# Kernel optimization log

Measured on AMD Instinct MI355X. Metric: run time of the kernel, lower is better.

Reference implementation:

```python
import jax, jax.numpy as jnp
import numpy as np

FREQ = 129  # STFT_FILTERS // 2


def conv1d(x, w, b, stride, pad):
    # x: [B, Cin, L], w: [Cout, Cin, K] (torch Conv1d layout)
    out = jax.lax.conv_general_dilated(x, w, (stride,), [(pad, pad)],
                                       dimension_numbers=('NCH', 'OIH', 'NCH'))
    if b is not None:
        out = out + b[None, :, None]
    return out


def setup_inputs() -> dict:
    key = jax.random.key(0)
    ks = jax.random.split(key, 17)
    B = 16384
    s = 0.05
    return {
        'x': jax.random.normal(ks[0], (B, 512), jnp.float32),
        'state': jax.random.normal(ks[1], (2, B, 128), jnp.float32),
        'stft_w': jax.random.normal(ks[2], (258, 1, 256), jnp.float32) * s,
        'w1': jax.random.normal(ks[3], (128, 129, 3), jnp.float32) * s,
        'b1': jax.random.normal(ks[4], (128,), jnp.float32) * s,
        'w2': jax.random.normal(ks[5], (64, 128, 3), jnp.float32) * s,
        'b2': jax.random.normal(ks[6], (64,), jnp.float32) * s,
        'w3': jax.random.normal(ks[7], (64, 64, 3), jnp.float32) * s,
        'b3': jax.random.normal(ks[8], (64,), jnp.float32) * s,
        'w4': jax.random.normal(ks[9], (128, 64, 3), jnp.float32) * s,
        'b4': jax.random.normal(ks[10], (128,), jnp.float32) * s,
        'w_ih': jax.random.normal(ks[11], (512, 128), jnp.float32) * s,
        'w_hh': jax.random.normal(ks[12], (512, 128), jnp.float32) * s,
        'b_ih': jax.random.normal(ks[13], (512,), jnp.float32) * s,
        'b_hh': jax.random.normal(ks[14], (512,), jnp.float32) * s,
        'fw': jax.random.normal(ks[15], (1, 128, 1), jnp.float32) * s,
        'fb': jax.random.normal(ks[16], (1,), jnp.float32) * s,
    }


def reference(x, state, stft_w, w1, b1, w2, b2, w3, b3, w4, b4,
              w_ih, w_hh, b_ih, b_hh, fw, fb):
    # reflect-pad right by 64: [B, 512] -> [B, 576], add channel dim
    xp = jnp.pad(x, ((0, 0), (0, 64)), mode='reflect')[:, None, :]
    s = conv1d(xp, stft_w, None, 128, 0)            # [B, 258, 3]
    real, imag = s[:, :FREQ], s[:, FREQ:]
    h = jnp.sqrt(real * real + imag * imag)          # magnitude [B, 129, 3]
    h = jax.nn.relu(conv1d(h, w1, b1, 1, 1))         # [B, 128, 3]
    h = jax.nn.relu(conv1d(h, w2, b2, 2, 1))         # [B, 64, 2]
    h = jax.nn.relu(conv1d(h, w3, b3, 2, 1))         # [B, 64, 1]
    h = jax.nn.relu(conv1d(h, w4, b4, 1, 1))         # [B, 128, 1]
    feat = h[:, :, 0]                                # [B, 128]
    # torch LSTMCell: gate order i, f, g, o
    gates = feat @ w_ih.T + b_ih + state[0] @ w_hh.T + b_hh
    i, f, g, o = jnp.split(gates, 4, axis=1)
    c = jax.nn.sigmoid(f) * state[1] + jax.nn.sigmoid(i) * jnp.tanh(g)
    hn = jax.nn.sigmoid(o) * jnp.tanh(c)
    new_state = jnp.stack([hn, c], axis=0)           # [2, B, 128]
    z = jax.nn.relu(hn)[:, :, None]                  # [B, 128, 1]
    z = jax.nn.sigmoid(conv1d(z, fw, fb, 1, 0))      # [B, 1, 1]
    out = z[:, 0].mean(axis=1, keepdims=True)        # [B, 1]
    return out, new_state
```

## Files before the change

### kernel.cpp

```cpp
#include <hip/hip_runtime.h>
#include <math.h>

typedef unsigned short ushort_t;
typedef short short8 __attribute__((ext_vector_type(8)));
typedef float floatx4 __attribute__((ext_vector_type(4)));

#define MFMA16(a,b,c) __builtin_amdgcn_mfma_f32_16x16x32_bf16((a),(b),(c),0,0,0)

#define PK_STFT 0
#define PK_W1   69632
#define PK_W2   131072
#define PK_W3   155648
#define PK_W4   167936
#define PK_LSTM 176128
#define OFF_MAG 307200
#define OFF_FEAT 8171520

__device__ __forceinline__ ushort_t f2bf(float f){
    unsigned int u = __float_as_uint(f);
    u += 0x7fffu + ((u >> 16) & 1u);
    return (ushort_t)(u >> 16);
}
__device__ __forceinline__ float bf2f(ushort_t h){
    return __uint_as_float(((unsigned int)h) << 16);
}
__device__ __forceinline__ unsigned int pack2(float a, float b){
    return (unsigned int)f2bf(a) | ((unsigned int)f2bf(b) << 16);
}
__device__ __forceinline__ float fsig(float v){
    return __builtin_amdgcn_rcpf(1.f + __builtin_amdgcn_exp2f(-1.44269504f * v));
}
__device__ __forceinline__ float ftanh(float v){
    return 2.f * __builtin_amdgcn_rcpf(1.f + __builtin_amdgcn_exp2f(-2.88539008f * v)) - 1.f;
}

__global__ __launch_bounds__(256) void prep_kernel(
    const float* __restrict__ stft_w, const float* __restrict__ w1,
    const float* __restrict__ w2, const float* __restrict__ w3,
    const float* __restrict__ w4, const float* __restrict__ wih,
    const float* __restrict__ whh, ushort_t* __restrict__ wp)
{
    int i = blockIdx.x * 256 + threadIdx.x;
    if (i >= 307200) return;
    float val = 0.f;
    if (i < PK_W1) {
        int frag = i >> 9, rr = i & 511, l = rr >> 3, j = rr & 7;
        int ct = frag >> 3, kk = frag & 7;
        int kd = kk * 32 + ((l >> 4) << 3) + j;
        int n = ct * 16 + (l & 15);
        val = (n < 258) ? stft_w[n * 256 + kd] : 0.f;
    } else if (i < PK_W2) {
        int r = i - PK_W1;
        int tap = r / 20480; r -= tap * 20480;
        int frag = r >> 9, rr = r & 511, l = rr >> 3, j = rr & 7;
        int ct = frag / 5, kk = frag - ct * 5;
        int kd = kk * 32 + ((l >> 4) << 3) + j;
        int c = ct * 16 + (l & 15);
        val = (kd < 129) ? w1[c * 387 + kd * 3 + tap] : 0.f;
    } else if (i < PK_W3) {
        int r = i - PK_W2;
        int frag = r >> 9, rr = r & 511, l = rr >> 3, j = rr & 7;
        int ct = frag / 12, kk = frag - ct * 12;
        int kd = kk * 32 + ((l >> 4) << 3) + j;
        int k = kd >> 7, f = kd & 127;
        int c = ct * 16 + (l & 15);
        val = w2[c * 384 + f * 3 + k];
    } else if (i < PK_W4) {
        int r = i - PK_W3;
        int frag = r >> 9, rr = r & 511, l = rr >> 3, j = rr & 7;
        int ct = frag / 6, kk = frag - ct * 6;
        int kd = kk * 32 + ((l >> 4) << 3) + j;
        int k = kd >> 6, f = kd & 63;
        int c = ct * 16 + (l & 15);
        val = w3[c * 192 + f * 3 + k];
    } else if (i < PK_LSTM) {
        int r = i - PK_W4;
        int frag = r >> 9, rr = r & 511, l = rr >> 3, j = rr & 7;
        int ct = frag >> 1, kk = frag & 1;
        int kd = kk * 32 + ((l >> 4) << 3) + j;
        int c = ct * 16 + (l & 15);
        val = w4[c * 192 + kd * 3 + 1];
    } else {
        int r = i - PK_LSTM;
        int frag = r >> 9, rr = r & 511, l = rr >> 3, j = rr & 7;
        int ct = frag >> 3, kk = frag & 7;
        int kd = kk * 32 + ((l >> 4) << 3) + j;
        int n = ct * 16 + (l & 15);
        val = (kd < 128) ? wih[n * 128 + kd] : whh[n * 128 + (kd - 128)];
    }
    wp[i] = f2bf(val);
}

__global__ __launch_bounds__(256) void stft_kernel(
    const float* __restrict__ x, const ushort_t* __restrict__ wp,
    ushort_t* __restrict__ magg)
{
    __shared__ ushort_t xs[48 * 264];
    __shared__ ushort_t s[48 * 264];
    const int tid = threadIdx.x, lane = tid & 63, wid = tid >> 6;
    const int l15 = lane & 15, lk = lane >> 4;

    {
        const float4* xg = (const float4*)(x + (size_t)blockIdx.x * 16 * 512);
#pragma unroll
        for (int i = 0; i < 8; ++i) {
            int idx4 = tid + i * 256;
            float4 v = xg[idx4];
            int b = idx4 >> 7, c4 = idx4 & 127;
            int si = c4 * 4, t1 = si >> 7;
            unsigned int u0 = pack2(v.x, v.y), u1 = pack2(v.z, v.w);
            if (t1 < 3) {
                ushort_t* p = &xs[(b * 3 + t1) * 264 + (si & 127)];
                *(unsigned int*)p = u0; *(unsigned int*)(p + 2) = u1;
            }
            if (t1 >= 1) {
                ushort_t* p = &xs[(b * 3 + t1 - 1) * 264 + (si & 127) + 128];
                *(unsigned int*)p = u0; *(unsigned int*)(p + 2) = u1;
            }
        }
    }
    __syncthreads();

    for (int ct = wid; ct < 17; ct += 4) {
        short8 bfrag[8];
        const short8* bp = (const short8*)(wp + PK_STFT) + (size_t)(ct * 8) * 64 + lane;
#pragma unroll
        for (int kk = 0; kk < 8; ++kk) bfrag[kk] = bp[kk * 64];
        int col = ct * 16 + l15;
#pragma unroll
        for (int rt = 0; rt < 3; ++rt) {
            const ushort_t* abase = &xs[(rt * 16 + l15) * 264 + lk * 8];
            floatx4 acc = {0.f, 0.f, 0.f, 0.f};
#pragma unroll
            for (int kk = 0; kk < 8; ++kk) {
                short8 af = *(const short8*)(abase + kk * 32);
                acc = MFMA16(af, bfrag[kk], acc);
            }
            if (col < 258) {
                int r0 = rt * 16 + lk * 4;
#pragma unroll
                for (int jj = 0; jj < 4; ++jj) s[(r0 + jj) * 264 + col] = f2bf(acc[jj]);
            }
        }
    }
    __syncthreads();

    {
        size_t ob = (size_t)blockIdx.x * 16 * 480;
        for (int idx = tid; idx < 48 * 129; idx += 256) {
            int bt = idx / 129, f = idx - bt * 129;
            float re = bf2f(s[bt * 264 + f]);
            float im = bf2f(s[bt * 264 + 129 + f]);
            int b = bt / 3, t = bt - b * 3;
            magg[ob + b * 480 + t * 160 + f] = f2bf(sqrtf(re * re + im * im));
        }
        for (int idx = tid; idx < 48 * 31; idx += 256) {
            int bt = idx / 31, f = 129 + (idx - bt * 31);
            int b = bt / 3, t = bt - b * 3;
            magg[ob + b * 480 + t * 160 + f] = 0;
        }
    }
}

__global__ __launch_bounds__(256) void conv_kernel(
    const ushort_t* __restrict__ wp, const ushort_t* __restrict__ magg,
    const float* __restrict__ b1, const float* __restrict__ b2,
    const float* __restrict__ b3, const float* __restrict__ b4,
    ushort_t* __restrict__ featg)
{
    __shared__ ushort_t big[13440];
    __shared__ ushort_t h2h[16 * 3 * 72];
    __shared__ ushort_t h3s[16 * 72];
    const int tid = threadIdx.x, lane = tid & 63, wid = tid >> 6;
    const int l15 = lane & 15, lk = lane >> 4;

    {
        unsigned int* bz = (unsigned int*)big;
        for (int i = tid; i < 2688; i += 256) {
            int bb = i / 168, r = i - bb * 168;
            int tp = (r < 84) ? 0 : 4, f2 = (r < 84) ? r : r - 84;
            bz[(bb * 5 + tp) * 84 + f2] = 0u;
        }
        for (int i = tid; i < 576; i += 256) {
            int bb = i / 36, f2 = i - bb * 36;
            ((unsigned int*)h2h)[bb * 108 + f2] = 0u;
        }
        const unsigned int* mg = (const unsigned int*)(magg + (size_t)blockIdx.x * 16 * 480);
        for (int i = tid; i < 3840; i += 256) {
            int bb = i / 240, r = i - bb * 240;
            int t = r / 80, f2 = r - t * 80;
            bz[(bb * 5 + 1 + t) * 84 + f2] = mg[i];
        }
    }
    __syncthreads();

    floatx4 acc1[2][3];
#pragma unroll
    for (int ci = 0; ci < 2; ++ci)
#pragma unroll
        for (int rt = 0; rt < 3; ++rt) acc1[ci][rt] = (floatx4){0.f, 0.f, 0.f, 0.f};
#pragma unroll
    for (int ci = 0; ci < 2; ++ci) {
        int ct = wid + ci * 4;
        short8 bfrag[15];
#pragma unroll
        for (int tap = 0; tap < 3; ++tap)
#pragma unroll
            for (int kk = 0; kk < 5; ++kk)
                bfrag[tap * 5 + kk] = ((const short8*)(wp + PK_W1))[(size_t)(tap * 40 + ct * 5 + kk) * 64 + lane];
#pragma unroll
        for (int rt = 0; rt < 3; ++rt) {
            int obt = rt * 16 + l15;
            int b = obt / 3, t = obt - b * 3;
#pragma unroll
            for (int tap = 0; tap < 3; ++tap) {
                const ushort_t* abase = &big[(b * 5 + t + tap) * 168 + lk * 8];
#pragma unroll
                for (int kk = 0; kk < 5; ++kk) {
                    short8 af = *(const short8*)(abase + kk * 32);
                    acc1[ci][rt] = MFMA16(af, bfrag[tap * 5 + kk], acc1[ci][rt]);
                }
            }
        }
    }
    __syncthreads();

    {
        unsigned int* h1z = (unsigned int*)big;
        for (int i = tid; i < 2176; i += 256) {
            int bb = i / 136, r = i - bb * 136;
            int tp = (r < 68) ? 0 : 4, f2 = (r < 68) ? r : r - 68;
            h1z[(bb * 5 + tp) * 68 + f2] = 0u;
        }
#pragma unroll
        for (int ci = 0; ci < 2; ++ci) {
            int ct = wid + ci * 4;
            int col = ct * 16 + l15;
            float bias = b1[col];
#pragma unroll
            for (int rt = 0; rt < 3; ++rt)
#pragma unroll
                for (int jj = 0; jj < 4; ++jj) {
                    int obt = rt * 16 + lk * 4 + jj;
                    int b = obt / 3, t = obt - b * 3;
                    big[(b * 5 + t + 1) * 136 + col] = f2bf(fmaxf(acc1[ci][rt][jj] + bias, 0.f));
                }
        }
    }
    __syncthreads();

    {
        int ct = wid;
        short8 bfrag[12];
#pragma unroll
        for (int kk = 0; kk < 12; ++kk)
            bfrag[kk] = ((const short8*)(wp + PK_W2))[(size_t)(ct * 12 + kk) * 64 + lane];
        int col = ct * 16 + l15;
        float bias = b2[col];
#pragma unroll
        for (int rt = 0; rt < 2; ++rt) {
            floatx4 acc = {0.f, 0.f, 0.f, 0.f};
            int orow = rt * 16 + l15;
            int b = orow >> 1, t2 = orow & 1;
#pragma unroll
            for (int kk = 0; kk < 12; ++kk) {
                int k = kk >> 2, f = (kk & 3) * 32 + lk * 8;
                short8 af = *(const short8*)(&big[(b * 5 + 2 * t2 + k) * 136 + f]);
                acc = MFMA16(af, bfrag[kk], acc);
            }
#pragma unroll
            for (int jj = 0; jj < 4; ++jj) {
                int orw = rt * 16 + lk * 4 + jj;
                int bb = orw >> 1, tt = orw & 1;
                h2h[(bb * 3 + 1 + tt) * 72 + col] = f2bf(fmaxf(acc[jj] + bias, 0.f));
            }
        }
    }
    __syncthreads();

    {
        int ct = wid;
        short8 bfrag[6];
#pragma unroll
        for (int kk = 0; kk < 6; ++kk)
            bfrag[kk] = ((const short8*)(wp + PK_W3))[(size_t)(ct * 6 + kk) * 64 + lane];
        int col = ct * 16 + l15;
        float bias = b3[col];
        floatx4 acc = {0.f, 0.f, 0.f, 0.f};
        int b = l15;
#pragma unroll
        for (int kk = 0; kk < 6; ++kk) {
            int k = kk >> 1, f = (kk & 1) * 32 + lk * 8;
            short8 af = *(const short8*)(&h2h[(b * 3 + k) * 72 + f]);
            acc = MFMA16(af, bfrag[kk], acc);
        }
#pragma unroll
        for (int jj = 0; jj < 4; ++jj) {
            int bb = lk * 4 + jj;
            h3s[bb * 72 + col] = f2bf(fmaxf(acc[jj] + bias, 0.f));
        }
    }
    __syncthreads();

    {
#pragma unroll
        for (int ci = 0; ci < 2; ++ci) {
            int ct = wid + ci * 4;
            short8 bf0 = ((const short8*)(wp + PK_W4))[(size_t)(ct * 2 + 0) * 64 + lane];
            short8 bf1 = ((const short8*)(wp + PK_W4))[(size_t)(ct * 2 + 1) * 64 + lane];
            int col = ct * 16 + l15;
            float bias = b4[col];
            floatx4 acc = {0.f, 0.f, 0.f, 0.f};
            int b = l15;
            short8 a0 = *(const short8*)(&h3s[b * 72 + lk * 8]);
            short8 a1 = *(const short8*)(&h3s[b * 72 + 32 + lk * 8]);
            acc = MFMA16(a0, bf0, acc);
            acc = MFMA16(a1, bf1, acc);
#pragma unroll
            for (int jj = 0; jj < 4; ++jj) {
                int bb = lk * 4 + jj;
                featg[((size_t)blockIdx.x * 16 + bb) * 128 + col] = f2bf(fmaxf(acc[jj] + bias, 0.f));
            }
        }
    }
}

__global__ __launch_bounds__(512) void lstm_kernel(
    const ushort_t* __restrict__ featg, const float* __restrict__ state,
    const ushort_t* __restrict__ wp, const float* __restrict__ bih,
    const float* __restrict__ bhh, const float* __restrict__ fw,
    const float* __restrict__ fbp, float* __restrict__ out, int B)
{
    __shared__ ushort_t inc[32 * 264];
    __shared__ float red[256];
    const int tid = threadIdx.x, lane = tid & 63, wid = tid >> 6;
    const int l15 = lane & 15, lk = lane >> 4;
    const size_t b0 = (size_t)blockIdx.x * 32;
    const int cc = wid * 16 + l15;

    const float* cprev = state + (size_t)B * 128;
    float cpv[2][4];
#pragma unroll
    for (int rt = 0; rt < 2; ++rt)
#pragma unroll
        for (int jj = 0; jj < 4; ++jj)
            cpv[rt][jj] = cprev[(b0 + rt * 16 + lk * 4 + jj) * 128 + cc];

    {
        const unsigned int* fg = (const unsigned int*)(featg + b0 * 128);
        unsigned int* ip = (unsigned int*)inc;
        for (int i = tid; i < 2048; i += 512) {
            int bb = i >> 6, f2 = i & 63;
            ip[bb * 132 + f2] = fg[i];
        }
        const float* hp = state + b0 * 128;
        for (int i = tid; i < 2048; i += 512) {
            int bb = i >> 6, c2 = i & 63;
            float2 v = *(const float2*)&hp[bb * 128 + c2 * 2];
            ip[bb * 132 + 64 + c2] = pack2(v.x, v.y);
        }
    }
    __syncthreads();

    floatx4 acc[4][2];
#pragma unroll
    for (int ci = 0; ci < 4; ++ci) {
        int ct = wid + ci * 8;
        short8 bfrag[8];
#pragma unroll
        for (int kk = 0; kk < 8; ++kk)
            bfrag[kk] = ((const short8*)(wp + PK_LSTM))[(size_t)(ct * 8 + kk) * 64 + lane];
#pragma unroll
        for (int rt = 0; rt < 2; ++rt) {
            const ushort_t* abase = &inc[(rt * 16 + l15) * 264 + lk * 8];
            floatx4 a = {0.f, 0.f, 0.f, 0.f};
#pragma unroll
            for (int kk = 0; kk < 8; ++kk) {
                short8 af = *(const short8*)(abase + kk * 32);
                a = MFMA16(af, bfrag[kk], a);
            }
            acc[ci][rt] = a;
        }
    }

    float* outh = out + B;
    float* outc = out + B + (size_t)B * 128;
    float ph[2][4];
    const float bi = bih[cc] + bhh[cc];
    const float bf_ = bih[cc + 128] + bhh[cc + 128];
    const float bg = bih[cc + 256] + bhh[cc + 256];
    const float bo = bih[cc + 384] + bhh[cc + 384];
    const float fwv = fw[cc];
#pragma unroll
    for (int rt = 0; rt < 2; ++rt)
#pragma unroll
        for (int jj = 0; jj < 4; ++jj) {
            int row = rt * 16 + lk * 4 + jj;
            size_t gb = b0 + row;
            float gi = acc[0][rt][jj] + bi;
            float gf = acc[1][rt][jj] + bf_;
            float gg = acc[2][rt][jj] + bg;
            float go = acc[3][rt][jj] + bo;
            float cn = fsig(gf) * cpv[rt][jj] + fsig(gi) * ftanh(gg);
            float hn = fsig(go) * ftanh(cn);
            outh[gb * 128 + cc] = hn;
            outc[gb * 128 + cc] = cn;
            ph[rt][jj] = fmaxf(hn, 0.f) * fwv;
        }

#pragma unroll
    for (int rt = 0; rt < 2; ++rt)
#pragma unroll
        for (int jj = 0; jj < 4; ++jj) {
            float v = ph[rt][jj];
            v += __shfl_xor(v, 1, 64);
            v += __shfl_xor(v, 2, 64);
            v += __shfl_xor(v, 4, 64);
            v += __shfl_xor(v, 8, 64);
            if (l15 == 0) red[wid * 32 + rt * 16 + lk * 4 + jj] = v;
        }
    __syncthreads();
    if (tid < 32) {
        float v = 0.f;
#pragma unroll
        for (int w = 0; w < 8; ++w) v += red[w * 32 + tid];
        out[b0 + tid] = fsig(v + fbp[0]);
    }
}

extern "C" void kernel_launch(void* const* d_in, const int* in_sizes, int n_in,
                              void* d_out, int out_size, void* d_ws, size_t ws_size,
                              hipStream_t stream) {
    const float* x      = (const float*)d_in[0];
    const float* state  = (const float*)d_in[1];
    const float* stft_w = (const float*)d_in[2];
    const float* w1     = (const float*)d_in[3];
    const float* b1     = (const float*)d_in[4];
    const float* w2     = (const float*)d_in[5];
    const float* b2     = (const float*)d_in[6];
    const float* w3     = (const float*)d_in[7];
    const float* b3     = (const float*)d_in[8];
    const float* w4     = (const float*)d_in[9];
    const float* b4     = (const float*)d_in[10];
    const float* wih    = (const float*)d_in[11];
    const float* whh    = (const float*)d_in[12];
    const float* bih    = (const float*)d_in[13];
    const float* bhh    = (const float*)d_in[14];
    const float* fw     = (const float*)d_in[15];
    const float* fbp    = (const float*)d_in[16];

    ushort_t* wp = (ushort_t*)d_ws;
    const int B = in_sizes[0] / 512;

    prep_kernel<<<1200, 256, 0, stream>>>(stft_w, w1, w2, w3, w4, wih, whh, wp);
    stft_kernel<<<B / 16, 256, 0, stream>>>(x, wp, wp + OFF_MAG);
    conv_kernel<<<B / 16, 256, 0, stream>>>(wp, wp + OFF_MAG, b1, b2, b3, b4, wp + OFF_FEAT);
    lstm_kernel<<<B / 32, 512, 0, stream>>>(wp + OFF_FEAT, state, wp, bih, bhh, fw, fbp,
                                            (float*)d_out, B);
}
```

Baseline: 73.69 us.

## Fuse STFT, conv stack and LSTM into one per-16-row kernel

Merges the three separate kernels (STFT magnitude, conv stack, LSTM cell) into one block-per-16-batch-rows kernel. Magnitude and feature intermediates stay in shared memory instead of going through global workspace buffers. The previous hidden and cell state are prefetched into registers before the STFT work starts. This removes global round trips and two launches, but the kernel uses more registers and LDS (launch bounds set to 3 blocks per SM). The LSTM GEMM now runs per 16-row tile with half the batch rows per block, so its weight fragments are reloaded twice as often.

```diff
diff --git a/kernel.cpp b/kernel.cpp
--- a/kernel.cpp
+++ b/kernel.cpp
@@ -13,8 +13,6 @@
 #define PK_W3   155648
 #define PK_W4   167936
 #define PK_LSTM 176128
-#define OFF_MAG 307200
-#define OFF_FEAT 8171520
 
 __device__ __forceinline__ ushort_t f2bf(float f){
     unsigned int u = __float_as_uint(f);
@@ -91,17 +89,26 @@
     wp[i] = f2bf(val);
 }
 
-__global__ __launch_bounds__(256) void stft_kernel(
-    const float* __restrict__ x, const ushort_t* __restrict__ wp,
-    ushort_t* __restrict__ magg)
+__global__ __launch_bounds__(256, 3) void fused_kernel(
+    const float* __restrict__ x, const float* __restrict__ state,
+    const ushort_t* __restrict__ wp,
+    const float* __restrict__ b1, const float* __restrict__ b2,
+    const float* __restrict__ b3, const float* __restrict__ b4,
+    const float* __restrict__ bih, const float* __restrict__ bhh,
+    const float* __restrict__ fw, const float* __restrict__ fbp,
+    float* __restrict__ out, int B)
 {
-    __shared__ ushort_t xs[48 * 264];
-    __shared__ ushort_t s[48 * 264];
+    __shared__ ushort_t A[12672];
+    __shared__ ushort_t Bb[13440];
+    __shared__ float red[64];
+
     const int tid = threadIdx.x, lane = tid & 63, wid = tid >> 6;
     const int l15 = lane & 15, lk = lane >> 4;
-
-    {
-        const float4* xg = (const float4*)(x + (size_t)blockIdx.x * 16 * 512);
+    const size_t b0 = (size_t)blockIdx.x * 16;
+
+    for (int i = tid; i < 6720; i += 256) ((unsigned int*)Bb)[i] = 0u;
+    {
+        const float4* xg = (const float4*)(x + b0 * 512);
 #pragma unroll
         for (int i = 0; i < 8; ++i) {
             int idx4 = tid + i * 256;
@@ -110,87 +117,87 @@
             int si = c4 * 4, t1 = si >> 7;
             unsigned int u0 = pack2(v.x, v.y), u1 = pack2(v.z, v.w);
             if (t1 < 3) {
-                ushort_t* p = &xs[(b * 3 + t1) * 264 + (si & 127)];
+                ushort_t* p = &A[(b * 3 + t1) * 264 + (si & 127)];
                 *(unsigned int*)p = u0; *(unsigned int*)(p + 2) = u1;
             }
             if (t1 >= 1) {
-                ushort_t* p = &xs[(b * 3 + t1 - 1) * 264 + (si & 127) + 128];
+                ushort_t* p = &A[(b * 3 + t1 - 1) * 264 + (si & 127) + 128];
                 *(unsigned int*)p = u0; *(unsigned int*)(p + 2) = u1;
             }
         }
     }
-    __syncthreads();
-
-    for (int ct = wid; ct < 17; ct += 4) {
-        short8 bfrag[8];
-        const short8* bp = (const short8*)(wp + PK_STFT) + (size_t)(ct * 8) * 64 + lane;
-#pragma unroll
-        for (int kk = 0; kk < 8; ++kk) bfrag[kk] = bp[kk * 64];
-        int col = ct * 16 + l15;
-#pragma unroll
-        for (int rt = 0; rt < 3; ++rt) {
-            const ushort_t* abase = &xs[(rt * 16 + l15) * 264 + lk * 8];
-            floatx4 acc = {0.f, 0.f, 0.f, 0.f};
-#pragma unroll
-            for (int kk = 0; kk < 8; ++kk) {
-                short8 af = *(const short8*)(abase + kk * 32);
-                acc = MFMA16(af, bfrag[kk], acc);
-            }
+    unsigned int hpk[4];
+    {
+        const float* hp = state + b0 * 128;
+#pragma unroll
+        for (int k = 0; k < 4; ++k) {
+            int i = tid + k * 256;
+            int bb = i >> 6, c2 = i & 63;
+            float2 v = *(const float2*)&hp[bb * 128 + c2 * 2];
+            hpk[k] = pack2(v.x, v.y);
+        }
+    }
+    const float* cprev = state + (size_t)B * 128;
+    float cpv[2][4];
+#pragma unroll
+    for (int g2 = 0; g2 < 2; ++g2) {
+        int cc = (wid + g2 * 4) * 16 + l15;
+#pragma unroll
+        for (int jj = 0; jj < 4; ++jj)
+            cpv[g2][jj] = cprev[(b0 + lk * 4 + jj) * 128 + cc];
+    }
+    __syncthreads();
+
+    floatx4 accs[5][3];
+#pragma unroll
+    for (int ci = 0; ci < 5; ++ci)
+#pragma unroll
+        for (int rt = 0; rt < 3; ++rt) accs[ci][rt] = (floatx4){0.f, 0.f, 0.f, 0.f};
+#pragma unroll
+    for (int ci = 0; ci < 5; ++ci) {
+        int ct = wid + ci * 4;
+        if (ct < 17) {
+            short8 bfrag[8];
+            const short8* bp = (const short8*)(wp + PK_STFT) + (size_t)(ct * 8) * 64 + lane;
+#pragma unroll
+            for (int kk = 0; kk < 8; ++kk) bfrag[kk] = bp[kk * 64];
+#pragma unroll
+            for (int rt = 0; rt < 3; ++rt) {
+                const ushort_t* abase = &A[(rt * 16 + l15) * 264 + lk * 8];
+                floatx4 a = accs[ci][rt];
+#pragma unroll
+                for (int kk = 0; kk < 8; ++kk)
+                    a = MFMA16(*(const short8*)(abase + kk * 32), bfrag[kk], a);
+                accs[ci][rt] = a;
+            }
+        }
+    }
+    __syncthreads();
+
+#pragma unroll
+    for (int ci = 0; ci < 5; ++ci) {
+        int ct = wid + ci * 4;
+        if (ct < 17) {
+            int col = ct * 16 + l15;
             if (col < 258) {
-                int r0 = rt * 16 + lk * 4;
-#pragma unroll
-                for (int jj = 0; jj < 4; ++jj) s[(r0 + jj) * 264 + col] = f2bf(acc[jj]);
-            }
-        }
-    }
-    __syncthreads();
-
-    {
-        size_t ob = (size_t)blockIdx.x * 16 * 480;
-        for (int idx = tid; idx < 48 * 129; idx += 256) {
-            int bt = idx / 129, f = idx - bt * 129;
-            float re = bf2f(s[bt * 264 + f]);
-            float im = bf2f(s[bt * 264 + 129 + f]);
-            int b = bt / 3, t = bt - b * 3;
-            magg[ob + b * 480 + t * 160 + f] = f2bf(sqrtf(re * re + im * im));
-        }
-        for (int idx = tid; idx < 48 * 31; idx += 256) {
-            int bt = idx / 31, f = 129 + (idx - bt * 31);
-            int b = bt / 3, t = bt - b * 3;
-            magg[ob + b * 480 + t * 160 + f] = 0;
-        }
-    }
-}
-
-__global__ __launch_bounds__(256) void conv_kernel(
-    const ushort_t* __restrict__ wp, const ushort_t* __restrict__ magg,
-    const float* __restrict__ b1, const float* __restrict__ b2,
-    const float* __restrict__ b3, const float* __restrict__ b4,
-    ushort_t* __restrict__ featg)
-{
-    __shared__ ushort_t big[13440];
-    __shared__ ushort_t h2h[16 * 3 * 72];
-    __shared__ ushort_t h3s[16 * 72];
-    const int tid = threadIdx.x, lane = tid & 63, wid = tid >> 6;
-    const int l15 = lane & 15, lk = lane >> 4;
-
-    {
-        unsigned int* bz = (unsigned int*)big;
-        for (int i = tid; i < 2688; i += 256) {
-            int bb = i / 168, r = i - bb * 168;
-            int tp = (r < 84) ? 0 : 4, f2 = (r < 84) ? r : r - 84;
-            bz[(bb * 5 + tp) * 84 + f2] = 0u;
-        }
-        for (int i = tid; i < 576; i += 256) {
-            int bb = i / 36, f2 = i - bb * 36;
-            ((unsigned int*)h2h)[bb * 108 + f2] = 0u;
-        }
-        const unsigned int* mg = (const unsigned int*)(magg + (size_t)blockIdx.x * 16 * 480);
-        for (int i = tid; i < 3840; i += 256) {
-            int bb = i / 240, r = i - bb * 240;
-            int t = r / 80, f2 = r - t * 80;
-            bz[(bb * 5 + 1 + t) * 84 + f2] = mg[i];
-        }
+#pragma unroll
+                for (int rt = 0; rt < 3; ++rt) {
+                    int r0 = rt * 16 + lk * 4;
+#pragma unroll
+                    for (int jj = 0; jj < 4; ++jj)
+                        A[(r0 + jj) * 264 + col] = f2bf(accs[ci][rt][jj]);
+                }
+            }
+        }
+    }
+    __syncthreads();
+
+    for (int idx = tid; idx < 6192; idx += 256) {
+        int bt = idx / 129, f = idx - bt * 129;
+        float re = bf2f(A[bt * 264 + f]);
+        float im = bf2f(A[bt * 264 + 129 + f]);
+        int b = bt / 3, t = bt - b * 3;
+        Bb[b * 840 + (1 + t) * 168 + f] = f2bf(sqrtf(re * re + im * im));
     }
     __syncthreads();
 
@@ -214,28 +221,29 @@
             int b = obt / 3, t = obt - b * 3;
 #pragma unroll
             for (int tap = 0; tap < 3; ++tap) {
-                const ushort_t* abase = &big[(b * 5 + t + tap) * 168 + lk * 8];
-#pragma unroll
-                for (int kk = 0; kk < 5; ++kk) {
-                    short8 af = *(const short8*)(abase + kk * 32);
-                    acc1[ci][rt] = MFMA16(af, bfrag[tap * 5 + kk], acc1[ci][rt]);
-                }
-            }
-        }
-    }
-    __syncthreads();
-
-    {
-        unsigned int* h1z = (unsigned int*)big;
+                const ushort_t* abase = &Bb[(b * 5 + t + tap) * 168 + lk * 8];
+#pragma unroll
+                for (int kk = 0; kk < 5; ++kk)
+                    acc1[ci][rt] = MFMA16(*(const short8*)(abase + kk * 32), bfrag[tap * 5 + kk], acc1[ci][rt]);
+            }
+        }
+    }
+    __syncthreads();
+
+    {
+        unsigned int* h1z = (unsigned int*)A;
         for (int i = tid; i < 2176; i += 256) {
             int bb = i / 136, r = i - bb * 136;
             int tp = (r < 68) ? 0 : 4, f2 = (r < 68) ? r : r - 68;
             h1z[(bb * 5 + tp) * 68 + f2] = 0u;
         }
+        for (int i = tid; i < 576; i += 256) {
+            int bb = i / 36, f2 = i - bb * 36;
+            ((unsigned int*)Bb)[bb * 108 + f2] = 0u;
+        }
 #pragma unroll
         for (int ci = 0; ci < 2; ++ci) {
-            int ct = wid + ci * 4;
-            int col = ct * 16 + l15;
+            int ct = wid + ci * 4, col = ct * 16 + l15;
             float bias = b1[col];
 #pragma unroll
             for (int rt = 0; rt < 3; ++rt)
@@ -243,7 +251,7 @@
                 for (int jj = 0; jj < 4; ++jj) {
                     int obt = rt * 16 + lk * 4 + jj;
                     int b = obt / 3, t = obt - b * 3;
-                    big[(b * 5 + t + 1) * 136 + col] = f2bf(fmaxf(acc1[ci][rt][jj] + bias, 0.f));
+                    A[(b * 5 + t + 1) * 136 + col] = f2bf(fmaxf(acc1[ci][rt][jj] + bias, 0.f));
                 }
         }
     }
@@ -265,14 +273,14 @@
 #pragma unroll
             for (int kk = 0; kk < 12; ++kk) {
                 int k = kk >> 2, f = (kk & 3) * 32 + lk * 8;
-                short8 af = *(const short8*)(&big[(b * 5 + 2 * t2 + k) * 136 + f]);
+                short8 af = *(const short8*)(&A[(b * 5 + 2 * t2 + k) * 136 + f]);
                 acc = MFMA16(af, bfrag[kk], acc);
             }
 #pragma unroll
             for (int jj = 0; jj < 4; ++jj) {
                 int orw = rt * 16 + lk * 4 + jj;
                 int bb = orw >> 1, tt = orw & 1;
-                h2h[(bb * 3 + 1 + tt) * 72 + col] = f2bf(fmaxf(acc[jj] + bias, 0.f));
+                Bb[(bb * 3 + 1 + tt) * 72 + col] = f2bf(fmaxf(acc[jj] + bias, 0.f));
             }
         }
     }
@@ -291,14 +299,12 @@
 #pragma unroll
         for (int kk = 0; kk < 6; ++kk) {
             int k = kk >> 1, f = (kk & 1) * 32 + lk * 8;
-            short8 af = *(const short8*)(&h2h[(b * 3 + k) * 72 + f]);
+            short8 af = *(const short8*)(&Bb[(b * 3 + k) * 72 + f]);
             acc = MFMA16(af, bfrag[kk], acc);
         }
 #pragma unroll
-        for (int jj = 0; jj < 4; ++jj) {
-            int bb = lk * 4 + jj;
-            h3s[bb * 72 + col] = f2bf(fmaxf(acc[jj] + bias, 0.f));
-        }
+        for (int jj = 0; jj < 4; ++jj)
+            A[(lk * 4 + jj) * 72 + col] = f2bf(fmaxf(acc[jj] + bias, 0.f));
     }
     __syncthreads();
 
@@ -312,118 +318,78 @@
             float bias = b4[col];
             floatx4 acc = {0.f, 0.f, 0.f, 0.f};
             int b = l15;
-            short8 a0 = *(const short8*)(&h3s[b * 72 + lk * 8]);
-            short8 a1 = *(const short8*)(&h3s[b * 72 + 32 + lk * 8]);
+            short8 a0 = *(const short8*)(&A[b * 72 + lk * 8]);
+            short8 a1 = *(const short8*)(&A[b * 72 + 32 + lk * 8]);
             acc = MFMA16(a0, bf0, acc);
             acc = MFMA16(a1, bf1, acc);
 #pragma unroll
             for (int jj = 0; jj < 4; ++jj) {
                 int bb = lk * 4 + jj;
-                featg[((size_t)blockIdx.x * 16 + bb) * 128 + col] = f2bf(fmaxf(acc[jj] + bias, 0.f));
-            }
-        }
-    }
-}
-
-__global__ __launch_bounds__(512) void lstm_kernel(
-    const ushort_t* __restrict__ featg, const float* __restrict__ state,
-    const ushort_t* __restrict__ wp, const float* __restrict__ bih,
-    const float* __restrict__ bhh, const float* __restrict__ fw,
-    const float* __restrict__ fbp, float* __restrict__ out, int B)
-{
-    __shared__ ushort_t inc[32 * 264];
-    __shared__ float red[256];
-    const int tid = threadIdx.x, lane = tid & 63, wid = tid >> 6;
-    const int l15 = lane & 15, lk = lane >> 4;
-    const size_t b0 = (size_t)blockIdx.x * 32;
-    const int cc = wid * 16 + l15;
-
-    const float* cprev = state + (size_t)B * 128;
-    float cpv[2][4];
-#pragma unroll
-    for (int rt = 0; rt < 2; ++rt)
-#pragma unroll
-        for (int jj = 0; jj < 4; ++jj)
-            cpv[rt][jj] = cprev[(b0 + rt * 16 + lk * 4 + jj) * 128 + cc];
-
-    {
-        const unsigned int* fg = (const unsigned int*)(featg + b0 * 128);
-        unsigned int* ip = (unsigned int*)inc;
-        for (int i = tid; i < 2048; i += 512) {
-            int bb = i >> 6, f2 = i & 63;
-            ip[bb * 132 + f2] = fg[i];
-        }
-        const float* hp = state + b0 * 128;
-        for (int i = tid; i < 2048; i += 512) {
+                Bb[bb * 264 + col] = f2bf(fmaxf(acc[jj] + bias, 0.f));
+            }
+        }
+#pragma unroll
+        for (int k = 0; k < 4; ++k) {
+            int i = tid + k * 256;
             int bb = i >> 6, c2 = i & 63;
-            float2 v = *(const float2*)&hp[bb * 128 + c2 * 2];
-            ip[bb * 132 + 64 + c2] = pack2(v.x, v.y);
-        }
-    }
-    __syncthreads();
-
-    floatx4 acc[4][2];
-#pragma unroll
-    for (int ci = 0; ci < 4; ++ci) {
-        int ct = wid + ci * 8;
+            *(unsigned int*)&Bb[bb * 264 + 128 + c2 * 2] = hpk[k];
+        }
+    }
+    __syncthreads();
+
+    floatx4 acg[8];
+#pragma unroll
+    for (int ci = 0; ci < 8; ++ci) {
+        int ct = wid + ci * 4;
         short8 bfrag[8];
 #pragma unroll
         for (int kk = 0; kk < 8; ++kk)
             bfrag[kk] = ((const short8*)(wp + PK_LSTM))[(size_t)(ct * 8 + kk) * 64 + lane];
-#pragma unroll
-        for (int rt = 0; rt < 2; ++rt) {
-            const ushort_t* abase = &inc[(rt * 16 + l15) * 264 + lk * 8];
-            floatx4 a = {0.f, 0.f, 0.f, 0.f};
-#pragma unroll
-            for (int kk = 0; kk < 8; ++kk) {
-                short8 af = *(const short8*)(abase + kk * 32);
-                a = MFMA16(af, bfrag[kk], a);
-            }
-            acc[ci][rt] = a;
-        }
+        const ushort_t* abase = &Bb[l15 * 264 + lk * 8];
+        floatx4 a = {0.f, 0.f, 0.f, 0.f};
+#pragma unroll
+        for (int kk = 0; kk < 8; ++kk)
+            a = MFMA16(*(const short8*)(abase + kk * 32), bfrag[kk], a);
+        acg[ci] = a;
     }
 
     float* outh = out + B;
     float* outc = out + B + (size_t)B * 128;
-    float ph[2][4];
-    const float bi = bih[cc] + bhh[cc];
-    const float bf_ = bih[cc + 128] + bhh[cc + 128];
-    const float bg = bih[cc + 256] + bhh[cc + 256];
-    const float bo = bih[cc + 384] + bhh[cc + 384];
-    const float fwv = fw[cc];
-#pragma unroll
-    for (int rt = 0; rt < 2; ++rt)
+    float phs[4] = {0.f, 0.f, 0.f, 0.f};
+#pragma unroll
+    for (int g2 = 0; g2 < 2; ++g2) {
+        int cc = (wid + g2 * 4) * 16 + l15;
+        float bi = bih[cc] + bhh[cc];
+        float bf_ = bih[cc + 128] + bhh[cc + 128];
+        float bg = bih[cc + 256] + bhh[cc + 256];
+        float bo = bih[cc + 384] + bhh[cc + 384];
+        float fwv = fw[cc];
 #pragma unroll
         for (int jj = 0; jj < 4; ++jj) {
-            int row = rt * 16 + lk * 4 + jj;
-            size_t gb = b0 + row;
-            float gi = acc[0][rt][jj] + bi;
-            float gf = acc[1][rt][jj] + bf_;
-            float gg = acc[2][rt][jj] + bg;
-            float go = acc[3][rt][jj] + bo;
-            float cn = fsig(gf) * cpv[rt][jj] + fsig(gi) * ftanh(gg);
+            size_t gb = b0 + lk * 4 + jj;
+            float gi = acg[g2][jj] + bi;
+            float gf = acg[g2 + 2][jj] + bf_;
+            float gg = acg[g2 + 4][jj] + bg;
+            float go = acg[g2 + 6][jj] + bo;
+            float cn = fsig(gf) * cpv[g2][jj] + fsig(gi) * ftanh(gg);
             float hn = fsig(go) * ftanh(cn);
             outh[gb * 128 + cc] = hn;
             outc[gb * 128 + cc] = cn;
-            ph[rt][jj] = fmaxf(hn, 0.f) * fwv;
-        }
-
-#pragma unroll
-    for (int rt = 0; rt < 2; ++rt)
-#pragma unroll
-        for (int jj = 0; jj < 4; ++jj) {
-            float v = ph[rt][jj];
-            v += __shfl_xor(v, 1, 64);
-            v += __shfl_xor(v, 2, 64);
-            v += __shfl_xor(v, 4, 64);
-            v += __shfl_xor(v, 8, 64);
-            if (l15 == 0) red[wid * 32 + rt * 16 + lk * 4 + jj] = v;
-        }
-    __syncthreads();
-    if (tid < 32) {
-        float v = 0.f;
-#pragma unroll
-        for (int w = 0; w < 8; ++w) v += red[w * 32 + tid];
+            phs[jj] += fmaxf(hn, 0.f) * fwv;
+        }
+    }
+#pragma unroll
+    for (int jj = 0; jj < 4; ++jj) {
+        float v = phs[jj];
+        v += __shfl_xor(v, 1, 64);
+        v += __shfl_xor(v, 2, 64);
+        v += __shfl_xor(v, 4, 64);
+        v += __shfl_xor(v, 8, 64);
+        if (l15 == 0) red[wid * 16 + lk * 4 + jj] = v;
+    }
+    __syncthreads();
+    if (tid < 16) {
+        float v = red[tid] + red[16 + tid] + red[32 + tid] + red[48 + tid];
         out[b0 + tid] = fsig(v + fbp[0]);
     }
 }
@@ -453,8 +419,6 @@
     const int B = in_sizes[0] / 512;
 
     prep_kernel<<<1200, 256, 0, stream>>>(stft_w, w1, w2, w3, w4, wih, whh, wp);
-    stft_kernel<<<B / 16, 256, 0, stream>>>(x, wp, wp + OFF_MAG);
-    conv_kernel<<<B / 16, 256, 0, stream>>>(wp, wp + OFF_MAG, b1, b2, b3, b4, wp + OFF_FEAT);
-    lstm_kernel<<<B / 32, 512, 0, stream>>>(wp + OFF_FEAT, state, wp, bih, bhh, fw, fbp,
-                                            (float*)d_out, B);
-}
+    fused_kernel<<<B / 16, 256, 0, stream>>>(x, state, wp, b1, b2, b3, b4,
+                                             bih, bhh, fw, fbp, (float*)d_out, B);
+}
```

New measurement: 114.5 us. +55.4%, slower.

## Stage kernel outputs through shared memory for coalesced global loads and stores

Applied to the files above, without the earlier changes.

The STFT magnitude and conv feature outputs are now written to shared memory first and then copied to global memory as contiguous 32-bit words. The LSTM kernel loads the previous cell state coalesced into LDS, and stages h and c results in LDS before coalesced global stores. Occupancy hints are added to launch bounds. This replaces scattered strided global accesses with coalesced ones, at the cost of extra barriers and more LDS use, which may reduce occupancy.

```diff
diff --git a/kernel.cpp b/kernel.cpp
--- a/kernel.cpp
+++ b/kernel.cpp
@@ -91,7 +91,7 @@
     wp[i] = f2bf(val);
 }
 
-__global__ __launch_bounds__(256) void stft_kernel(
+__global__ __launch_bounds__(256, 3) void stft_kernel(
     const float* __restrict__ x, const ushort_t* __restrict__ wp,
     ushort_t* __restrict__ magg)
 {
@@ -146,19 +146,26 @@
     __syncthreads();
 
     {
-        size_t ob = (size_t)blockIdx.x * 16 * 480;
+        ushort_t* ml = xs;
         for (int idx = tid; idx < 48 * 129; idx += 256) {
             int bt = idx / 129, f = idx - bt * 129;
             float re = bf2f(s[bt * 264 + f]);
             float im = bf2f(s[bt * 264 + 129 + f]);
             int b = bt / 3, t = bt - b * 3;
-            magg[ob + b * 480 + t * 160 + f] = f2bf(sqrtf(re * re + im * im));
+            ml[b * 480 + t * 160 + f] = f2bf(sqrtf(re * re + im * im));
         }
         for (int idx = tid; idx < 48 * 31; idx += 256) {
             int bt = idx / 31, f = 129 + (idx - bt * 31);
             int b = bt / 3, t = bt - b * 3;
-            magg[ob + b * 480 + t * 160 + f] = 0;
-        }
+            ml[b * 480 + t * 160 + f] = 0;
+        }
+    }
+    __syncthreads();
+    {
+        unsigned int* mgd = (unsigned int*)(magg + (size_t)blockIdx.x * 16 * 480);
+        const unsigned int* mls = (const unsigned int*)xs;
+#pragma unroll
+        for (int k = 0; k < 15; ++k) mgd[tid + k * 256] = mls[tid + k * 256];
     }
 }
 
@@ -303,6 +310,7 @@
     __syncthreads();
 
     {
+        ushort_t* fbuf = h2h;
 #pragma unroll
         for (int ci = 0; ci < 2; ++ci) {
             int ct = wid + ci * 4;
@@ -319,32 +327,31 @@
 #pragma unroll
             for (int jj = 0; jj < 4; ++jj) {
                 int bb = lk * 4 + jj;
-                featg[((size_t)blockIdx.x * 16 + bb) * 128 + col] = f2bf(fmaxf(acc[jj] + bias, 0.f));
-            }
-        }
-    }
-}
-
-__global__ __launch_bounds__(512) void lstm_kernel(
+                fbuf[bb * 128 + col] = f2bf(fmaxf(acc[jj] + bias, 0.f));
+            }
+        }
+        __syncthreads();
+        unsigned int* fgd = (unsigned int*)(featg + (size_t)blockIdx.x * 16 * 128);
+        const unsigned int* fls = (const unsigned int*)fbuf;
+#pragma unroll
+        for (int k = 0; k < 4; ++k) fgd[tid + k * 256] = fls[tid + k * 256];
+    }
+}
+
+__global__ __launch_bounds__(512, 6) void lstm_kernel(
     const ushort_t* __restrict__ featg, const float* __restrict__ state,
     const ushort_t* __restrict__ wp, const float* __restrict__ bih,
     const float* __restrict__ bhh, const float* __restrict__ fw,
     const float* __restrict__ fbp, float* __restrict__ out, int B)
 {
     __shared__ ushort_t inc[32 * 264];
+    __shared__ float cpl[32 * 132];
     __shared__ float red[256];
     const int tid = threadIdx.x, lane = tid & 63, wid = tid >> 6;
     const int l15 = lane & 15, lk = lane >> 4;
     const size_t b0 = (size_t)blockIdx.x * 32;
     const int cc = wid * 16 + l15;
-
     const float* cprev = state + (size_t)B * 128;
-    float cpv[2][4];
-#pragma unroll
-    for (int rt = 0; rt < 2; ++rt)
-#pragma unroll
-        for (int jj = 0; jj < 4; ++jj)
-            cpv[rt][jj] = cprev[(b0 + rt * 16 + lk * 4 + jj) * 128 + cc];
 
     {
         const unsigned int* fg = (const unsigned int*)(featg + b0 * 128);
@@ -353,11 +360,16 @@
             int bb = i >> 6, f2 = i & 63;
             ip[bb * 132 + f2] = fg[i];
         }
-        const float* hp = state + b0 * 128;
+        const float2* hp2 = (const float2*)(state + b0 * 128);
         for (int i = tid; i < 2048; i += 512) {
             int bb = i >> 6, c2 = i & 63;
-            float2 v = *(const float2*)&hp[bb * 128 + c2 * 2];
+            float2 v = hp2[i];
             ip[bb * 132 + 64 + c2] = pack2(v.x, v.y);
+        }
+        const float* cg = cprev + b0 * 128;
+        for (int i = tid; i < 4096; i += 512) {
+            int bb = i >> 7, c = i & 127;
+            cpl[bb * 132 + c] = cg[i];
         }
     }
     __syncthreads();
@@ -382,29 +394,29 @@
             acc[ci][rt] = a;
         }
     }
-
-    float* outh = out + B;
-    float* outc = out + B + (size_t)B * 128;
-    float ph[2][4];
+    __syncthreads();
+
+    float* hsl = (float*)inc;
+    float* csl = cpl;
     const float bi = bih[cc] + bhh[cc];
     const float bf_ = bih[cc + 128] + bhh[cc + 128];
     const float bg = bih[cc + 256] + bhh[cc + 256];
     const float bo = bih[cc + 384] + bhh[cc + 384];
     const float fwv = fw[cc];
+    float ph[2][4];
 #pragma unroll
     for (int rt = 0; rt < 2; ++rt)
 #pragma unroll
         for (int jj = 0; jj < 4; ++jj) {
             int row = rt * 16 + lk * 4 + jj;
-            size_t gb = b0 + row;
             float gi = acc[0][rt][jj] + bi;
             float gf = acc[1][rt][jj] + bf_;
             float gg = acc[2][rt][jj] + bg;
             float go = acc[3][rt][jj] + bo;
-            float cn = fsig(gf) * cpv[rt][jj] + fsig(gi) * ftanh(gg);
+            float cn = fsig(gf) * cpl[row * 132 + cc] + fsig(gi) * ftanh(gg);
             float hn = fsig(go) * ftanh(cn);
-            outh[gb * 128 + cc] = hn;
-            outc[gb * 128 + cc] = cn;
+            hsl[row * 132 + cc] = hn;
+            csl[row * 132 + cc] = cn;
             ph[rt][jj] = fmaxf(hn, 0.f) * fwv;
         }
 
@@ -420,6 +432,16 @@
             if (l15 == 0) red[wid * 32 + rt * 16 + lk * 4 + jj] = v;
         }
     __syncthreads();
+
+    {
+        float* outh = out + B + b0 * 128;
+        float* outc = out + B + (size_t)B * 128 + b0 * 128;
+        for (int i = tid; i < 4096; i += 512) {
+            int bb = i >> 7, c = i & 127;
+            outh[i] = hsl[bb * 132 + c];
+            outc[i] = csl[bb * 132 + c];
+        }
+    }
     if (tid < 32) {
         float v = 0.f;
 #pragma unroll
```

New measurement: 80.78 us. +9.6%, slower.

## Interleave STFT real/imag columns and compute magnitude in registers via lane shuffle

Applied to the files above, without the earlier changes.

The STFT weight packing is reordered so the real and imaginary outputs of each frequency land in adjacent MFMA columns. The kernel now keeps all accumulators in registers, pairs real and imaginary values with a lane xor-shuffle, and computes the magnitude directly. The bf16 intermediate spectrum buffer in shared memory is removed. The magnitude tile is staged in the reused input buffer and written out with coalesced 32-bit stores. This removes a shared-memory round trip, a bf16 rounding of the intermediate spectrum, and the strided global magnitude writes, at the cost of more live accumulator registers.

```diff
diff --git a/kernel.cpp b/kernel.cpp
--- a/kernel.cpp
+++ b/kernel.cpp
@@ -48,7 +48,9 @@
         int ct = frag >> 3, kk = frag & 7;
         int kd = kk * 32 + ((l >> 4) << 3) + j;
         int n = ct * 16 + (l & 15);
-        val = (n < 258) ? stft_w[n * 256 + kd] : 0.f;
+        int f = n >> 1;
+        int ch = (n & 1) ? (129 + f) : f;
+        val = (n < 258) ? stft_w[ch * 256 + kd] : 0.f;
     } else if (i < PK_W2) {
         int r = i - PK_W1;
         int tap = r / 20480; r -= tap * 20480;
@@ -96,7 +98,6 @@
     ushort_t* __restrict__ magg)
 {
     __shared__ ushort_t xs[48 * 264];
-    __shared__ ushort_t s[48 * 264];
     const int tid = threadIdx.x, lane = tid & 63, wid = tid >> 6;
     const int l15 = lane & 15, lk = lane >> 4;
 
@@ -121,44 +122,67 @@
     }
     __syncthreads();
 
-    for (int ct = wid; ct < 17; ct += 4) {
-        short8 bfrag[8];
-        const short8* bp = (const short8*)(wp + PK_STFT) + (size_t)(ct * 8) * 64 + lane;
-#pragma unroll
-        for (int kk = 0; kk < 8; ++kk) bfrag[kk] = bp[kk * 64];
-        int col = ct * 16 + l15;
-#pragma unroll
-        for (int rt = 0; rt < 3; ++rt) {
-            const ushort_t* abase = &xs[(rt * 16 + l15) * 264 + lk * 8];
-            floatx4 acc = {0.f, 0.f, 0.f, 0.f};
-#pragma unroll
-            for (int kk = 0; kk < 8; ++kk) {
-                short8 af = *(const short8*)(abase + kk * 32);
-                acc = MFMA16(af, bfrag[kk], acc);
-            }
-            if (col < 258) {
-                int r0 = rt * 16 + lk * 4;
-#pragma unroll
-                for (int jj = 0; jj < 4; ++jj) s[(r0 + jj) * 264 + col] = f2bf(acc[jj]);
-            }
-        }
-    }
-    __syncthreads();
-
-    {
-        size_t ob = (size_t)blockIdx.x * 16 * 480;
-        for (int idx = tid; idx < 48 * 129; idx += 256) {
-            int bt = idx / 129, f = idx - bt * 129;
-            float re = bf2f(s[bt * 264 + f]);
-            float im = bf2f(s[bt * 264 + 129 + f]);
-            int b = bt / 3, t = bt - b * 3;
-            magg[ob + b * 480 + t * 160 + f] = f2bf(sqrtf(re * re + im * im));
-        }
-        for (int idx = tid; idx < 48 * 31; idx += 256) {
-            int bt = idx / 31, f = 129 + (idx - bt * 31);
-            int b = bt / 3, t = bt - b * 3;
-            magg[ob + b * 480 + t * 160 + f] = 0;
-        }
+    floatx4 accs[5][3];
+#pragma unroll
+    for (int ci = 0; ci < 5; ++ci)
+#pragma unroll
+        for (int rt = 0; rt < 3; ++rt) accs[ci][rt] = (floatx4){0.f, 0.f, 0.f, 0.f};
+#pragma unroll
+    for (int ci = 0; ci < 5; ++ci) {
+        int ct = wid + ci * 4;
+        if (ct < 17) {
+            short8 bfrag[8];
+            const short8* bp = (const short8*)(wp + PK_STFT) + (size_t)(ct * 8) * 64 + lane;
+#pragma unroll
+            for (int kk = 0; kk < 8; ++kk) bfrag[kk] = bp[kk * 64];
+#pragma unroll
+            for (int rt = 0; rt < 3; ++rt) {
+                const ushort_t* abase = &xs[(rt * 16 + l15) * 264 + lk * 8];
+                floatx4 a = accs[ci][rt];
+#pragma unroll
+                for (int kk = 0; kk < 8; ++kk)
+                    a = MFMA16(*(const short8*)(abase + kk * 32), bfrag[kk], a);
+                accs[ci][rt] = a;
+            }
+        }
+    }
+    __syncthreads();
+
+    {
+        ushort_t* ml = xs;
+        for (int r = tid; r < 48; r += 256) ml[r * 160 + 129] = 0;
+        for (int idx = tid; idx < 48 * 15; idx += 256) {
+            int r = idx / 15, d = idx - r * 15;
+            *(unsigned int*)&ml[r * 160 + 130 + d * 2] = 0u;
+        }
+#pragma unroll
+        for (int ci = 0; ci < 5; ++ci) {
+            int ct = wid + ci * 4;
+            if (ct < 17) {
+                int f = (ct * 16 + l15) >> 1;
+                bool wr = ((l15 & 1) == 0) && (f <= 128);
+#pragma unroll
+                for (int rt = 0; rt < 3; ++rt) {
+#pragma unroll
+                    for (int jj = 0; jj < 4; ++jj) {
+                        float v = accs[ci][rt][jj];
+                        float o = __shfl_xor(v, 1, 64);
+                        if (wr) {
+                            int row = rt * 16 + lk * 4 + jj;
+                            ml[row * 160 + f] = f2bf(sqrtf(v * v + o * o));
+                        }
+                    }
+                }
+            }
+        }
+    }
+    __syncthreads();
+
+    {
+        unsigned int* mgd = (unsigned int*)(magg + (size_t)blockIdx.x * 16 * 480);
+        const unsigned int* mls = (const unsigned int*)xs;
+#pragma unroll
+        for (int k = 0; k < 15; ++k) mgd[tid + k * 256] = mls[tid + k * 256];
     }
 }
 
```

Result: slower. 84.82 us (+15.1%).
